# Performance work log

Hardware: AMD Instinct MI355X
Metric: run time of the kernel (lower is better)

Reference implementation:

```python
import jax, jax.numpy as jnp
import numpy as np

V, E, T, H, L, FF = 32000, 512, 2048, 8, 6, 2048
B = 2
HD = E // H
EPS = 1e-5


def setup_inputs() -> dict:
    key = jax.random.key(0)
    ks = iter(jax.random.split(key, 32))
    s = 0.02
    d = {
        "x": jax.random.randint(next(ks), (B, T), 0, V),
        "tok_emb": jax.random.normal(next(ks), (V, E), jnp.float32) * s,
        "pos_emb": jax.random.normal(next(ks), (T, E), jnp.float32) * s,
        "Wq": jax.random.normal(next(ks), (L, E, E), jnp.float32) * s,
        "bq": jnp.zeros((L, E), jnp.float32),
        "Wk": jax.random.normal(next(ks), (L, E, E), jnp.float32) * s,
        "bk": jnp.zeros((L, E), jnp.float32),
        "Wv": jax.random.normal(next(ks), (L, E, E), jnp.float32) * s,
        "bv": jnp.zeros((L, E), jnp.float32),
        "Wo": jax.random.normal(next(ks), (L, E, E), jnp.float32) * s,
        "bo": jnp.zeros((L, E), jnp.float32),
        "ln1_s": jnp.ones((L, E), jnp.float32),
        "ln1_b": jnp.zeros((L, E), jnp.float32),
        "ln2_s": jnp.ones((L, E), jnp.float32),
        "ln2_b": jnp.zeros((L, E), jnp.float32),
        "W1": jax.random.normal(next(ks), (L, E, FF), jnp.float32) * s,
        "b1": jnp.zeros((L, FF), jnp.float32),
        "W2": jax.random.normal(next(ks), (L, FF, E), jnp.float32) * s,
        "b2": jnp.zeros((L, E), jnp.float32),
        "Wout": jax.random.normal(next(ks), (E, V), jnp.float32) * s,
        "bout": jnp.zeros((V,), jnp.float32),
    }
    return d


def _layernorm(x, scale, bias):
    mu = jnp.mean(x, axis=-1, keepdims=True)
    var = jnp.var(x, axis=-1, keepdims=True)
    return (x - mu) * jax.lax.rsqrt(var + EPS) * scale + bias


def reference(x, tok_emb, pos_emb, Wq, bq, Wk, bk, Wv, bv, Wo, bo,
              ln1_s, ln1_b, ln2_s, ln2_b, W1, b1, W2, b2, Wout, bout):
    b, t = x.shape
    h = tok_emb[x] + pos_emb[:t][None]  # [b,t,E]
    causal = jnp.tril(jnp.ones((t, t), bool))  # True on/below diag
    for i in range(L):
        y = _layernorm(h, ln1_s[i], ln1_b[i])
        q = (y @ Wq[i] + bq[i]).reshape(b, t, H, HD)
        k = (y @ Wk[i] + bk[i]).reshape(b, t, H, HD)
        v = (y @ Wv[i] + bv[i]).reshape(b, t, H, HD)
        scores = jnp.einsum("bqhd,bkhd->bhqk", q, k) / np.sqrt(HD).astype(np.float32)
        scores = jnp.where(causal, scores, -jnp.inf)
        attn = jax.nn.softmax(scores, axis=-1)
        o = jnp.einsum("bhqk,bkhd->bqhd", attn, v).reshape(b, t, E)
        h = h + (o @ Wo[i] + bo[i])  # dropout is identity at eval
        y = _layernorm(h, ln2_s[i], ln2_b[i])
        ff = jax.nn.relu(y @ W1[i] + b1[i]) @ W2[i] + b2[i]
        h = h + ff
    return h @ Wout + bout  # [b,t,V]
```

## Files before the change

### kernel.cpp

```cpp
#include <hip/hip_runtime.h>
#include <cstdint>
#include <cstddef>

#define TOKENS 4096
#define E_ 512
#define T_ 2048
#define H_ 8
#define L_ 6
#define FF_ 2048
#define V_ 32000

typedef unsigned short u16;
typedef __attribute__((ext_vector_type(8))) short short8;
typedef __attribute__((ext_vector_type(4))) float f32x4;

__device__ __forceinline__ u16 f2b(float f) {
  union { float f; unsigned u; } x; x.f = f;
  unsigned r = x.u + 0x7fffu + ((x.u >> 16) & 1u);
  return (u16)(r >> 16);
}

__device__ __forceinline__ void gload_lds16(const void* g, void* l) {
  __builtin_amdgcn_global_load_lds((__attribute__((address_space(1))) void*)(uintptr_t)g,
                                   (__attribute__((address_space(3))) void*)l, 16, 0, 0);
}

template<int BF16OUT, int RESID, int RELU>
__global__ __launch_bounds__(256) void gemm_bt(
    const u16* __restrict__ A, const u16* __restrict__ BT,
    const float* __restrict__ bias, const float* __restrict__ resid,
    void* __restrict__ outp, int M, int N, int K, int ldc)
{
  __shared__ u16 a_sm[128 * 32];
  __shared__ u16 b_sm[128 * 32];
  const int tid  = threadIdx.x;
  const int wave = tid >> 6;
  const int lane = tid & 63;
  const int l16  = lane & 15;
  const int quad = lane >> 4;
  const int bm = blockIdx.y << 7;
  const int bn = blockIdx.x << 7;
  const int wr = (wave >> 1) << 6;
  const int wc = (wave & 1) << 6;

  const int srow = tid >> 2;
  const int soff = (tid & 3) << 3;
  const u16* ag0 = A  + (size_t)(bm + srow) * K + soff;
  const u16* ag1 = A  + (size_t)(bm + 64 + srow) * K + soff;
  const u16* bg0 = BT + (size_t)(bn + srow) * K + soff;
  const u16* bg1 = BT + (size_t)(bn + 64 + srow) * K + soff;
  u16* al0 = a_sm + wave * 512;
  u16* al1 = a_sm + 2048 + wave * 512;
  u16* bl0 = b_sm + wave * 512;
  u16* bl1 = b_sm + 2048 + wave * 512;

  f32x4 acc[4][4] = {};

  for (int k0 = 0; k0 < K; k0 += 32) {
    gload_lds16(ag0 + k0, al0);
    gload_lds16(ag1 + k0, al1);
    gload_lds16(bg0 + k0, bl0);
    gload_lds16(bg1 + k0, bl1);
    __syncthreads();
    short8 af[4], bf[4];
#pragma unroll
    for (int mt = 0; mt < 4; ++mt)
      af[mt] = *(const short8*)&a_sm[(wr + mt * 16 + l16) * 32 + quad * 8];
#pragma unroll
    for (int nt = 0; nt < 4; ++nt)
      bf[nt] = *(const short8*)&b_sm[(wc + nt * 16 + l16) * 32 + quad * 8];
#pragma unroll
    for (int mt = 0; mt < 4; ++mt)
#pragma unroll
      for (int nt = 0; nt < 4; ++nt)
        acc[mt][nt] = __builtin_amdgcn_mfma_f32_16x16x32_bf16(af[mt], bf[nt], acc[mt][nt], 0, 0, 0);
    __syncthreads();
  }

#pragma unroll
  for (int mt = 0; mt < 4; ++mt) {
#pragma unroll
    for (int nt = 0; nt < 4; ++nt) {
      const int cg = bn + wc + nt * 16 + l16;
      const int rg = bm + wr + mt * 16 + quad * 4;
      const float bv = bias[cg];
#pragma unroll
      for (int i = 0; i < 4; ++i) {
        float v = acc[mt][nt][i] + bv;
        size_t idx = (size_t)(rg + i) * ldc + cg;
        if (RESID) v += resid[idx];
        if (RELU)  v = fmaxf(v, 0.f);
        if (BF16OUT) ((u16*)outp)[idx] = f2b(v);
        else         ((float*)outp)[idx] = v;
      }
    }
  }
}

__global__ __launch_bounds__(256) void gemm_bt_sk(
    const u16* __restrict__ A, const u16* __restrict__ BT,
    float* __restrict__ part, int M, int N, int lda, int kLen)
{
  __shared__ u16 a_sm[128 * 32];
  __shared__ u16 b_sm[128 * 32];
  const int tid  = threadIdx.x;
  const int wave = tid >> 6;
  const int lane = tid & 63;
  const int l16  = lane & 15;
  const int quad = lane >> 4;
  const int bm = blockIdx.y << 7;
  const int bn = blockIdx.x << 7;
  const int wr = (wave >> 1) << 6;
  const int wc = (wave & 1) << 6;

  const u16* Ab = A  + (size_t)blockIdx.z * kLen;
  const u16* Bb = BT + (size_t)blockIdx.z * kLen;

  const int srow = tid >> 2;
  const int soff = (tid & 3) << 3;
  const u16* ag0 = Ab + (size_t)(bm + srow) * lda + soff;
  const u16* ag1 = Ab + (size_t)(bm + 64 + srow) * lda + soff;
  const u16* bg0 = Bb + (size_t)(bn + srow) * lda + soff;
  const u16* bg1 = Bb + (size_t)(bn + 64 + srow) * lda + soff;
  u16* al0 = a_sm + wave * 512;
  u16* al1 = a_sm + 2048 + wave * 512;
  u16* bl0 = b_sm + wave * 512;
  u16* bl1 = b_sm + 2048 + wave * 512;

  f32x4 acc[4][4] = {};

  for (int k0 = 0; k0 < kLen; k0 += 32) {
    gload_lds16(ag0 + k0, al0);
    gload_lds16(ag1 + k0, al1);
    gload_lds16(bg0 + k0, bl0);
    gload_lds16(bg1 + k0, bl1);
    __syncthreads();
    short8 af[4], bf[4];
#pragma unroll
    for (int mt = 0; mt < 4; ++mt)
      af[mt] = *(const short8*)&a_sm[(wr + mt * 16 + l16) * 32 + quad * 8];
#pragma unroll
    for (int nt = 0; nt < 4; ++nt)
      bf[nt] = *(const short8*)&b_sm[(wc + nt * 16 + l16) * 32 + quad * 8];
#pragma unroll
    for (int mt = 0; mt < 4; ++mt)
#pragma unroll
      for (int nt = 0; nt < 4; ++nt)
        acc[mt][nt] = __builtin_amdgcn_mfma_f32_16x16x32_bf16(af[mt], bf[nt], acc[mt][nt], 0, 0, 0);
    __syncthreads();
  }

  float* out = part + (size_t)blockIdx.z * M * N;
#pragma unroll
  for (int mt = 0; mt < 4; ++mt) {
#pragma unroll
    for (int nt = 0; nt < 4; ++nt) {
      const int cg = bn + wc + nt * 16 + l16;
      const int rg = bm + wr + mt * 16 + quad * 4;
#pragma unroll
      for (int i = 0; i < 4; ++i)
        out[(size_t)(rg + i) * N + cg] = acc[mt][nt][i];
    }
  }
}

__global__ __launch_bounds__(256) void attn_kernel(const u16* __restrict__ qkv,
                                                   u16* __restrict__ o)
{
  __shared__ u16 k_sm[64 * 64];
  __shared__ u16 vT_sm[64 * 64];
  __shared__ u16 p_sm[4 * 16 * 64];
  const int tid  = threadIdx.x;
  const int wave = tid >> 6;
  const int lane = tid & 63;
  const int l16  = lane & 15;
  const int quad = lane >> 4;
  const int j  = blockIdx.x;
  const int bh = blockIdx.y;
  const int b  = bh >> 3, h = bh & 7;
  const size_t base = (size_t)b * T_ * 1536;

  const int qrow = j * 64 + wave * 16 + l16;
  short8 aq[2];
#pragma unroll
  for (int half = 0; half < 2; ++half)
    aq[half] = *(const short8*)&qkv[base + (size_t)qrow * 1536 + h * 64 + half * 32 + quad * 8];

  f32x4 oacc[4] = {};
  float m_i[4] = {-INFINITY, -INFINITY, -INFINITY, -INFINITY};
  float l_i[4] = {0.f, 0.f, 0.f, 0.f};

  const int ksrc = ((tid & 7) ^ ((tid >> 3) & 7)) * 8;

  const int nkt = j + 1;
  for (int kt = 0; kt < nkt; ++kt) {
    __syncthreads();
    gload_lds16(qkv + base + (size_t)(kt * 64 + (tid >> 3)) * 1536 + 512 + h * 64 + ksrc,
                k_sm + wave * 512);
    gload_lds16(qkv + base + (size_t)(kt * 64 + 32 + (tid >> 3)) * 1536 + 512 + h * 64 + ksrc,
                k_sm + 2048 + wave * 512);
    {
      const int t = tid >> 2, d0 = (tid & 3) * 16;
      const u16* vp = &qkv[base + (size_t)(kt * 64 + t) * 1536 + 1024 + h * 64 + d0];
      short8 v0 = *(const short8*)vp;
      short8 v1 = *(const short8*)(vp + 8);
#pragma unroll
      for (int i = 0; i < 8; ++i) vT_sm[(d0 + i) * 64 + (t ^ (i << 3))] = (u16)v0[i];
#pragma unroll
      for (int i = 0; i < 8; ++i) vT_sm[(d0 + 8 + i) * 64 + (t ^ (i << 3))] = (u16)v1[i];
    }
    __syncthreads();

    f32x4 s[4] = {};
#pragma unroll
    for (int nt = 0; nt < 4; ++nt)
#pragma unroll
      for (int half = 0; half < 2; ++half) {
        short8 bk = *(const short8*)&k_sm[(nt * 16 + l16) * 64 +
                                          (((half * 4 + quad) ^ (l16 & 7)) << 3)];
        s[nt] = __builtin_amdgcn_mfma_f32_16x16x32_bf16(aq[half], bk, s[nt], 0, 0, 0);
      }
#pragma unroll
    for (int nt = 0; nt < 4; ++nt)
#pragma unroll
      for (int i = 0; i < 4; ++i) {
        const int col = kt * 64 + nt * 16 + l16;
        const int row = j * 64 + wave * 16 + quad * 4 + i;
        float sv = s[nt][i] * 0.125f;
        s[nt][i] = (col <= row) ? sv : -INFINITY;
      }
    float rm[4], mn[4], alpha[4], rs[4], p[4][4];
#pragma unroll
    for (int i = 0; i < 4; ++i)
      rm[i] = fmaxf(fmaxf(s[0][i], s[1][i]), fmaxf(s[2][i], s[3][i]));
#pragma unroll
    for (int off = 1; off < 16; off <<= 1)
#pragma unroll
      for (int i = 0; i < 4; ++i) rm[i] = fmaxf(rm[i], __shfl_xor(rm[i], off));
#pragma unroll
    for (int i = 0; i < 4; ++i) {
      mn[i] = fmaxf(m_i[i], rm[i]);
      alpha[i] = __expf(m_i[i] - mn[i]);
      m_i[i] = mn[i];
#pragma unroll
      for (int nt = 0; nt < 4; ++nt) p[nt][i] = __expf(s[nt][i] - mn[i]);
      rs[i] = (p[0][i] + p[1][i]) + (p[2][i] + p[3][i]);
    }
#pragma unroll
    for (int off = 1; off < 16; off <<= 1)
#pragma unroll
      for (int i = 0; i < 4; ++i) rs[i] += __shfl_xor(rs[i], off);
#pragma unroll
    for (int i = 0; i < 4; ++i) l_i[i] = l_i[i] * alpha[i] + rs[i];
#pragma unroll
    for (int nt = 0; nt < 4; ++nt)
#pragma unroll
      for (int i = 0; i < 4; ++i) oacc[nt][i] *= alpha[i];
    u16* pw = p_sm + wave * 1024;
#pragma unroll
    for (int i = 0; i < 4; ++i) {
      const int pr = quad * 4 + i;
#pragma unroll
      for (int nt = 0; nt < 4; ++nt)
        pw[pr * 64 + ((nt * 16 + l16) ^ ((pr & 7) << 3))] = f2b(p[nt][i]);
    }
    asm volatile("s_waitcnt lgkmcnt(0)" ::: "memory");
    short8 pf[2];
#pragma unroll
    for (int kh = 0; kh < 2; ++kh)
      pf[kh] = *(const short8*)&pw[l16 * 64 + (((kh * 4 + quad) ^ (l16 & 7)) << 3)];
#pragma unroll
    for (int nt = 0; nt < 4; ++nt)
#pragma unroll
      for (int kh = 0; kh < 2; ++kh) {
        short8 bv = *(const short8*)&vT_sm[(nt * 16 + l16) * 64 +
                                           (((kh * 4 + quad) ^ (l16 & 7)) << 3)];
        oacc[nt] = __builtin_amdgcn_mfma_f32_16x16x32_bf16(pf[kh], bv, oacc[nt], 0, 0, 0);
      }
  }
#pragma unroll
  for (int nt = 0; nt < 4; ++nt)
#pragma unroll
    for (int i = 0; i < 4; ++i) {
      const int row = j * 64 + wave * 16 + quad * 4 + i;
      const float ov = oacc[nt][i] / l_i[i];
      o[(size_t)(b * T_ + row) * 512 + h * 64 + nt * 16 + l16] = f2b(ov);
    }
}

__device__ __forceinline__ void ln_emit(float2 hv, const float* __restrict__ sc,
                                        const float* __restrict__ bi, int tid,
                                        unsigned* __restrict__ yrow)
{
  float s = hv.x + hv.y;
  float q = hv.x * hv.x + hv.y * hv.y;
  for (int off = 32; off; off >>= 1) { s += __shfl_down(s, off); q += __shfl_down(q, off); }
  __shared__ float red[8];
  const int wave = tid >> 6, lane = tid & 63;
  if (!lane) { red[wave] = s; red[4 + wave] = q; }
  __syncthreads();
  if (tid == 0) {
    float ts = 0, tq = 0;
    for (int w = 0; w < 4; ++w) { ts += red[w]; tq += red[4 + w]; }
    red[0] = ts; red[4] = tq;
  }
  __syncthreads();
  const float mu = red[0] * (1.f / 512.f);
  const float var = red[4] * (1.f / 512.f) - mu * mu;
  const float rstd = rsqrtf(var + 1e-5f);
  const float y0 = (hv.x - mu) * rstd * sc[tid * 2]     + bi[tid * 2];
  const float y1 = (hv.y - mu) * rstd * sc[tid * 2 + 1] + bi[tid * 2 + 1];
  yrow[tid] = ((unsigned)f2b(y1) << 16) | (unsigned)f2b(y0);
}

template<int NS, int DOLN>
__global__ __launch_bounds__(256) void resid_ln_kernel(
    const float* __restrict__ part, const float* __restrict__ bias,
    float* __restrict__ h, const float* __restrict__ sc,
    const float* __restrict__ bi, u16* __restrict__ y)
{
  const int row = blockIdx.x, tid = threadIdx.x;
  float2 hv = ((const float2*)(h + (size_t)row * 512))[tid];
  const float2 bv = ((const float2*)bias)[tid];
#pragma unroll
  for (int s = 0; s < NS; ++s) {
    const float2 pv = ((const float2*)(part + ((size_t)s * TOKENS + row) * 512))[tid];
    hv.x += pv.x; hv.y += pv.y;
  }
  hv.x += bv.x; hv.y += bv.y;
  ((float2*)(h + (size_t)row * 512))[tid] = hv;
  if (DOLN)
    ln_emit(hv, sc, bi, tid, (unsigned*)(y + (size_t)row * 512));
  else
    ((unsigned*)y)[(size_t)row * 256 + tid] = ((unsigned)f2b(hv.y) << 16) | (unsigned)f2b(hv.x);
}

__global__ __launch_bounds__(256) void embed_ln_kernel(const int* __restrict__ x,
                                                       const float* __restrict__ tok,
                                                       const float* __restrict__ pos,
                                                       const float* __restrict__ sc,
                                                       const float* __restrict__ bi,
                                                       float* __restrict__ h,
                                                       u16* __restrict__ y)
{
  const int row = blockIdx.x, tid = threadIdx.x;
  const int t = row & (T_ - 1);
  const int tk = x[row];
  const float2 a = ((const float2*)tok)[(size_t)tk * 256 + tid];
  const float2 p = ((const float2*)pos)[(size_t)t * 256 + tid];
  float2 hv = make_float2(a.x + p.x, a.y + p.y);
  ((float2*)(h + (size_t)row * 512))[tid] = hv;
  ln_emit(hv, sc, bi, tid, (unsigned*)(y + (size_t)row * 512));
}

__global__ void transW(const float* __restrict__ src, u16* __restrict__ dst,
                       int K, int N, long sStr, long dStr)
{
  __shared__ float tile[32][33];
  const int l = blockIdx.z;
  const float* S = src + (size_t)l * sStr;
  u16* D = dst + (size_t)l * dStr;
  const int n0 = blockIdx.x * 32, k0 = blockIdx.y * 32;
  const int tx = threadIdx.x, ty = threadIdx.y;
#pragma unroll
  for (int i = 0; i < 4; ++i)
    tile[ty + 8 * i][tx] = S[(size_t)(k0 + ty + 8 * i) * N + n0 + tx];
  __syncthreads();
#pragma unroll
  for (int i = 0; i < 4; ++i)
    D[(size_t)(n0 + ty + 8 * i) * K + k0 + tx] = f2b(tile[tx][ty + 8 * i]);
}

__global__ __launch_bounds__(256) void bias_cat_kernel(const float* __restrict__ bq,
                                                       const float* __restrict__ bk,
                                                       const float* __restrict__ bv,
                                                       float* __restrict__ o)
{
  const int i = blockIdx.x * 256 + threadIdx.x;
  if (i >= L_ * 1536) return;
  const int l = i / 1536, c = i % 1536;
  float v = (c < 512) ? bq[l * 512 + c] : (c < 1024) ? bk[l * 512 + c - 512] : bv[l * 512 + c - 1024];
  o[i] = v;
}

extern "C" void kernel_launch(void* const* d_in, const int* in_sizes, int n_in,
                              void* d_out, int out_size, void* d_ws, size_t ws_size,
                              hipStream_t stream) {
  const int*   x     = (const int*)d_in[0];
  const float* tok   = (const float*)d_in[1];
  const float* pos   = (const float*)d_in[2];
  const float* Wq    = (const float*)d_in[3];
  const float* bq    = (const float*)d_in[4];
  const float* Wk    = (const float*)d_in[5];
  const float* bk    = (const float*)d_in[6];
  const float* Wv    = (const float*)d_in[7];
  const float* bv    = (const float*)d_in[8];
  const float* Wo    = (const float*)d_in[9];
  const float* bo    = (const float*)d_in[10];
  const float* ln1s  = (const float*)d_in[11];
  const float* ln1b  = (const float*)d_in[12];
  const float* ln2s  = (const float*)d_in[13];
  const float* ln2b  = (const float*)d_in[14];
  const float* W1    = (const float*)d_in[15];
  const float* b1    = (const float*)d_in[16];
  const float* W2    = (const float*)d_in[17];
  const float* b2    = (const float*)d_in[18];
  const float* Wout  = (const float*)d_in[19];
  const float* bout  = (const float*)d_in[20];

  char* ws = (char*)d_ws;
  size_t off = 0;
  auto alloc = [&](size_t bytes) { char* p = ws + off; off += (bytes + 255) & ~(size_t)255; return p; };
  u16*   qkvT  = (u16*)alloc((size_t)L_ * 1536 * 512 * 2);
  u16*   WoT   = (u16*)alloc((size_t)L_ * 512 * 512 * 2);
  u16*   W1T   = (u16*)alloc((size_t)L_ * 2048 * 512 * 2);
  u16*   W2T   = (u16*)alloc((size_t)L_ * 512 * 2048 * 2);
  u16*   WoutT = (u16*)alloc((size_t)V_ * 512 * 2);
  float* bqkv  = (float*)alloc((size_t)L_ * 1536 * 4);
  float* h     = (float*)alloc((size_t)TOKENS * 512 * 4);
  u16*   y     = (u16*)alloc((size_t)TOKENS * 512 * 2);
  u16*   qkv   = (u16*)alloc((size_t)TOKENS * 1536 * 2);
  u16*   obuf  = (u16*)alloc((size_t)TOKENS * 512 * 2);
  u16*   ff    = (u16*)alloc((size_t)TOKENS * 2048 * 2);
  u16*   hb    = (u16*)alloc((size_t)TOKENS * 512 * 2);
  float* part  = (float*)alloc((size_t)4 * TOKENS * 512 * 4);
  (void)ws_size; (void)in_sizes; (void)n_in; (void)out_size;

  transW<<<dim3(16, 16, L_), dim3(32, 8), 0, stream>>>(Wq, qkvT,             512, 512, 512L * 512, 1536L * 512);
  transW<<<dim3(16, 16, L_), dim3(32, 8), 0, stream>>>(Wk, qkvT + 512 * 512, 512, 512, 512L * 512, 1536L * 512);
  transW<<<dim3(16, 16, L_), dim3(32, 8), 0, stream>>>(Wv, qkvT + 1024 * 512,512, 512, 512L * 512, 1536L * 512);
  transW<<<dim3(16, 16, L_), dim3(32, 8), 0, stream>>>(Wo, WoT,              512, 512, 512L * 512, 512L * 512);
  transW<<<dim3(64, 16, L_), dim3(32, 8), 0, stream>>>(W1, W1T,  512, 2048, 512L * 2048, 2048L * 512);
  transW<<<dim3(16, 64, L_), dim3(32, 8), 0, stream>>>(W2, W2T, 2048,  512, 2048L * 512, 512L * 2048);
  transW<<<dim3(1000, 16, 1), dim3(32, 8), 0, stream>>>(Wout, WoutT, 512, V_, 0, 0);
  bias_cat_kernel<<<36, 256, 0, stream>>>(bq, bk, bv, bqkv);

  embed_ln_kernel<<<TOKENS, 256, 0, stream>>>(x, tok, pos, ln1s, ln1b, h, y);

  for (int l = 0; l < L_; ++l) {
    gemm_bt<1, 0, 0><<<dim3(12, 32), 256, 0, stream>>>(
        y, qkvT + (size_t)l * 1536 * 512, bqkv + l * 1536, nullptr, qkv, TOKENS, 1536, 512, 1536);
    attn_kernel<<<dim3(32, 16), 256, 0, stream>>>(qkv, obuf);
    gemm_bt_sk<<<dim3(4, 32, 2), 256, 0, stream>>>(
        obuf, WoT + (size_t)l * 512 * 512, part, TOKENS, 512, 512, 256);
    resid_ln_kernel<2, 1><<<TOKENS, 256, 0, stream>>>(
        part, bo + l * 512, h, ln2s + l * 512, ln2b + l * 512, y);
    gemm_bt<1, 0, 1><<<dim3(16, 32), 256, 0, stream>>>(
        y, W1T + (size_t)l * 2048 * 512, b1 + l * 2048, nullptr, ff, TOKENS, 2048, 512, 2048);
    gemm_bt_sk<<<dim3(4, 32, 4), 256, 0, stream>>>(
        ff, W2T + (size_t)l * 512 * 2048, part, TOKENS, 512, 2048, 512);
    if (l < L_ - 1)
      resid_ln_kernel<4, 1><<<TOKENS, 256, 0, stream>>>(
          part, b2 + l * 512, h, ln1s + (l + 1) * 512, ln1b + (l + 1) * 512, y);
    else
      resid_ln_kernel<4, 0><<<TOKENS, 256, 0, stream>>>(
          part, b2 + l * 512, h, nullptr, nullptr, hb);
  }

  gemm_bt<0, 0, 0><<<dim3(250, 32), 256, 0, stream>>>(
      hb, WoutT, bout, nullptr, (float*)d_out, TOKENS, V_, 512, V_);
}
```

Baseline: 1.850 ms.

## Double-buffer LDS tiles in GEMM and attention kernels to overlap loads with MFMA

Both GEMM kernels and the attention kernel now keep two LDS buffers. The next K-slice (or K/V tile) is prefetched into the spare buffer while MFMAs run on the current one, which also drops one barrier per iteration. In attention, V for the next tile is held in registers during compute and transposed into the other buffer afterwards. The goal is to hide global-load latency behind matrix math, at the cost of doubled LDS use and extra registers, which may reduce occupancy.

```diff
diff --git a/kernel.cpp b/kernel.cpp
--- a/kernel.cpp
+++ b/kernel.cpp
@@ -31,8 +31,8 @@
     const float* __restrict__ bias, const float* __restrict__ resid,
     void* __restrict__ outp, int M, int N, int K, int ldc)
 {
-  __shared__ u16 a_sm[128 * 32];
-  __shared__ u16 b_sm[128 * 32];
+  __shared__ u16 a_sm[2][128 * 32];
+  __shared__ u16 b_sm[2][128 * 32];
   const int tid  = threadIdx.x;
   const int wave = tid >> 6;
   const int lane = tid & 63;
@@ -49,32 +49,34 @@
   const u16* ag1 = A  + (size_t)(bm + 64 + srow) * K + soff;
   const u16* bg0 = BT + (size_t)(bn + srow) * K + soff;
   const u16* bg1 = BT + (size_t)(bn + 64 + srow) * K + soff;
-  u16* al0 = a_sm + wave * 512;
-  u16* al1 = a_sm + 2048 + wave * 512;
-  u16* bl0 = b_sm + wave * 512;
-  u16* bl1 = b_sm + 2048 + wave * 512;
+
+  auto stage = [&](int buf, int k0) {
+    gload_lds16(ag0 + k0, a_sm[buf] + wave * 512);
+    gload_lds16(ag1 + k0, a_sm[buf] + 2048 + wave * 512);
+    gload_lds16(bg0 + k0, b_sm[buf] + wave * 512);
+    gload_lds16(bg1 + k0, b_sm[buf] + 2048 + wave * 512);
+  };
 
   f32x4 acc[4][4] = {};
-
-  for (int k0 = 0; k0 < K; k0 += 32) {
-    gload_lds16(ag0 + k0, al0);
-    gload_lds16(ag1 + k0, al1);
-    gload_lds16(bg0 + k0, bl0);
-    gload_lds16(bg1 + k0, bl1);
+  const int ksteps = K >> 5;
+  stage(0, 0);
+  int cur = 0;
+  for (int t = 0; t < ksteps; ++t) {
     __syncthreads();
+    if (t + 1 < ksteps) stage(cur ^ 1, (t + 1) << 5);
     short8 af[4], bf[4];
 #pragma unroll
     for (int mt = 0; mt < 4; ++mt)
-      af[mt] = *(const short8*)&a_sm[(wr + mt * 16 + l16) * 32 + quad * 8];
-#pragma unroll
-    for (int nt = 0; nt < 4; ++nt)
-      bf[nt] = *(const short8*)&b_sm[(wc + nt * 16 + l16) * 32 + quad * 8];
+      af[mt] = *(const short8*)&a_sm[cur][(wr + mt * 16 + l16) * 32 + quad * 8];
+#pragma unroll
+    for (int nt = 0; nt < 4; ++nt)
+      bf[nt] = *(const short8*)&b_sm[cur][(wc + nt * 16 + l16) * 32 + quad * 8];
 #pragma unroll
     for (int mt = 0; mt < 4; ++mt)
 #pragma unroll
       for (int nt = 0; nt < 4; ++nt)
         acc[mt][nt] = __builtin_amdgcn_mfma_f32_16x16x32_bf16(af[mt], bf[nt], acc[mt][nt], 0, 0, 0);
-    __syncthreads();
+    cur ^= 1;
   }
 
 #pragma unroll
@@ -101,8 +103,8 @@
     const u16* __restrict__ A, const u16* __restrict__ BT,
     float* __restrict__ part, int M, int N, int lda, int kLen)
 {
-  __shared__ u16 a_sm[128 * 32];
-  __shared__ u16 b_sm[128 * 32];
+  __shared__ u16 a_sm[2][128 * 32];
+  __shared__ u16 b_sm[2][128 * 32];
   const int tid  = threadIdx.x;
   const int wave = tid >> 6;
   const int lane = tid & 63;
@@ -122,32 +124,34 @@
   const u16* ag1 = Ab + (size_t)(bm + 64 + srow) * lda + soff;
   const u16* bg0 = Bb + (size_t)(bn + srow) * lda + soff;
   const u16* bg1 = Bb + (size_t)(bn + 64 + srow) * lda + soff;
-  u16* al0 = a_sm + wave * 512;
-  u16* al1 = a_sm + 2048 + wave * 512;
-  u16* bl0 = b_sm + wave * 512;
-  u16* bl1 = b_sm + 2048 + wave * 512;
+
+  auto stage = [&](int buf, int k0) {
+    gload_lds16(ag0 + k0, a_sm[buf] + wave * 512);
+    gload_lds16(ag1 + k0, a_sm[buf] + 2048 + wave * 512);
+    gload_lds16(bg0 + k0, b_sm[buf] + wave * 512);
+    gload_lds16(bg1 + k0, b_sm[buf] + 2048 + wave * 512);
+  };
 
   f32x4 acc[4][4] = {};
-
-  for (int k0 = 0; k0 < kLen; k0 += 32) {
-    gload_lds16(ag0 + k0, al0);
-    gload_lds16(ag1 + k0, al1);
-    gload_lds16(bg0 + k0, bl0);
-    gload_lds16(bg1 + k0, bl1);
+  const int ksteps = kLen >> 5;
+  stage(0, 0);
+  int cur = 0;
+  for (int t = 0; t < ksteps; ++t) {
     __syncthreads();
+    if (t + 1 < ksteps) stage(cur ^ 1, (t + 1) << 5);
     short8 af[4], bf[4];
 #pragma unroll
     for (int mt = 0; mt < 4; ++mt)
-      af[mt] = *(const short8*)&a_sm[(wr + mt * 16 + l16) * 32 + quad * 8];
-#pragma unroll
-    for (int nt = 0; nt < 4; ++nt)
-      bf[nt] = *(const short8*)&b_sm[(wc + nt * 16 + l16) * 32 + quad * 8];
+      af[mt] = *(const short8*)&a_sm[cur][(wr + mt * 16 + l16) * 32 + quad * 8];
+#pragma unroll
+    for (int nt = 0; nt < 4; ++nt)
+      bf[nt] = *(const short8*)&b_sm[cur][(wc + nt * 16 + l16) * 32 + quad * 8];
 #pragma unroll
     for (int mt = 0; mt < 4; ++mt)
 #pragma unroll
       for (int nt = 0; nt < 4; ++nt)
         acc[mt][nt] = __builtin_amdgcn_mfma_f32_16x16x32_bf16(af[mt], bf[nt], acc[mt][nt], 0, 0, 0);
-    __syncthreads();
+    cur ^= 1;
   }
 
   float* out = part + (size_t)blockIdx.z * M * N;
@@ -167,8 +171,8 @@
 __global__ __launch_bounds__(256) void attn_kernel(const u16* __restrict__ qkv,
                                                    u16* __restrict__ o)
 {
-  __shared__ u16 k_sm[64 * 64];
-  __shared__ u16 vT_sm[64 * 64];
+  __shared__ u16 k_sm[2][64 * 64];
+  __shared__ u16 vT_sm[2][64 * 64];
   __shared__ u16 p_sm[4 * 16 * 64];
   const int tid  = threadIdx.x;
   const int wave = tid >> 6;
@@ -191,33 +195,42 @@
   float l_i[4] = {0.f, 0.f, 0.f, 0.f};
 
   const int ksrc = ((tid & 7) ^ ((tid >> 3) & 7)) * 8;
+  auto stageK = [&](int kt, int buf) {
+    gload_lds16(qkv + base + (size_t)(kt * 64 + (tid >> 3)) * 1536 + 512 + h * 64 + ksrc,
+                k_sm[buf] + wave * 512);
+    gload_lds16(qkv + base + (size_t)(kt * 64 + 32 + (tid >> 3)) * 1536 + 512 + h * 64 + ksrc,
+                k_sm[buf] + 2048 + wave * 512);
+  };
+  const int vt = tid >> 2, vd0 = (tid & 3) * 16;
+  auto loadV = [&](int kt, short8* vr) {
+    const u16* vp = &qkv[base + (size_t)(kt * 64 + vt) * 1536 + 1024 + h * 64 + vd0];
+    vr[0] = *(const short8*)vp;
+    vr[1] = *(const short8*)(vp + 8);
+  };
+  auto writeV = [&](int buf, const short8* vr) {
+#pragma unroll
+    for (int i = 0; i < 8; ++i) vT_sm[buf][(vd0 + i) * 64 + (vt ^ (i << 3))] = (u16)vr[0][i];
+#pragma unroll
+    for (int i = 0; i < 8; ++i) vT_sm[buf][(vd0 + 8 + i) * 64 + (vt ^ (i << 3))] = (u16)vr[1][i];
+  };
 
   const int nkt = j + 1;
+  short8 vr[2], vrn[2];
+  stageK(0, 0);
+  loadV(0, vr);
+  writeV(0, vr);
+  int cur = 0;
   for (int kt = 0; kt < nkt; ++kt) {
     __syncthreads();
-    gload_lds16(qkv + base + (size_t)(kt * 64 + (tid >> 3)) * 1536 + 512 + h * 64 + ksrc,
-                k_sm + wave * 512);
-    gload_lds16(qkv + base + (size_t)(kt * 64 + 32 + (tid >> 3)) * 1536 + 512 + h * 64 + ksrc,
-                k_sm + 2048 + wave * 512);
-    {
-      const int t = tid >> 2, d0 = (tid & 3) * 16;
-      const u16* vp = &qkv[base + (size_t)(kt * 64 + t) * 1536 + 1024 + h * 64 + d0];
-      short8 v0 = *(const short8*)vp;
-      short8 v1 = *(const short8*)(vp + 8);
-#pragma unroll
-      for (int i = 0; i < 8; ++i) vT_sm[(d0 + i) * 64 + (t ^ (i << 3))] = (u16)v0[i];
-#pragma unroll
-      for (int i = 0; i < 8; ++i) vT_sm[(d0 + 8 + i) * 64 + (t ^ (i << 3))] = (u16)v1[i];
-    }
-    __syncthreads();
+    if (kt + 1 < nkt) { stageK(kt + 1, cur ^ 1); loadV(kt + 1, vrn); }
 
     f32x4 s[4] = {};
 #pragma unroll
     for (int nt = 0; nt < 4; ++nt)
 #pragma unroll
       for (int half = 0; half < 2; ++half) {
-        short8 bk = *(const short8*)&k_sm[(nt * 16 + l16) * 64 +
-                                          (((half * 4 + quad) ^ (l16 & 7)) << 3)];
+        short8 bk = *(const short8*)&k_sm[cur][(nt * 16 + l16) * 64 +
+                                              (((half * 4 + quad) ^ (l16 & 7)) << 3)];
         s[nt] = __builtin_amdgcn_mfma_f32_16x16x32_bf16(aq[half], bk, s[nt], 0, 0, 0);
       }
 #pragma unroll
@@ -273,10 +286,13 @@
     for (int nt = 0; nt < 4; ++nt)
 #pragma unroll
       for (int kh = 0; kh < 2; ++kh) {
-        short8 bv = *(const short8*)&vT_sm[(nt * 16 + l16) * 64 +
-                                           (((kh * 4 + quad) ^ (l16 & 7)) << 3)];
+        short8 bv = *(const short8*)&vT_sm[cur][(nt * 16 + l16) * 64 +
+                                               (((kh * 4 + quad) ^ (l16 & 7)) << 3)];
         oacc[nt] = __builtin_amdgcn_mfma_f32_16x16x32_bf16(pf[kh], bv, oacc[nt], 0, 0, 0);
       }
+
+    if (kt + 1 < nkt) writeV(cur ^ 1, vrn);
+    cur ^= 1;
   }
 #pragma unroll
   for (int nt = 0; nt < 4; ++nt)
```

After: 1.836 ms. About the same (-0.8%).
